# Kernel optimization log

Hardware: AMD Instinct MI355X
Metric: run time of the kernel (lower is better)

The kernel has to match this reference:

```python
import jax, jax.numpy as jnp
import numpy as np

NODE_NUM = 200000   # full-graph embedding table rows
N = 100000          # batch_node_num (unique nodes in batch)
E_RAND = 1_600_000  # random edges (~16/node); self-loops appended -> E = 1.7M
IN_DIM = 256
OUT_DIM = 128
B = 50000           # query nodes
SLOPE = 0.1         # leaky_relu slope_ratio


def setup_inputs() -> dict:
    key = jax.random.key(0)
    k1, k2, k3, k4, k5, k6 = jax.random.split(key, 6)
    features = jax.random.normal(k1, (NODE_NUM, IN_DIM), dtype=jnp.float32)
    W = jax.random.normal(k2, (OUT_DIM, IN_DIM), dtype=jnp.float32) * 0.05
    b = jnp.zeros((OUT_DIM,), dtype=jnp.float32)
    a = jax.random.normal(k3, (2 * OUT_DIM, 1), dtype=jnp.float32) * 0.05
    er = jax.random.randint(k4, (E_RAND, 2), 0, N, dtype=jnp.int64)
    loops = jnp.stack([jnp.arange(N, dtype=jnp.int64)] * 2, axis=1)  # self-loops (original_node_edge)
    edges = jnp.concatenate([er, loops], axis=0)  # [E,2] (src, dst) in unique-node ids
    unique_nodes = jax.random.randint(k5, (N,), 0, NODE_NUM, dtype=jnp.int64)
    node_idx = jax.random.randint(k6, (B,), 0, N, dtype=jnp.int64)
    return {"features": features, "W": W, "b": b, "a": a,
            "edges": edges, "unique_nodes": unique_nodes, "node_idx": node_idx}


def reference(features, W, b, a, edges, unique_nodes, node_idx):
    # new_embeddings = out_linear_layer(features(n2))  -> [N, OUT]
    h = features[unique_nodes] @ W.T + b
    # score per edge: concat(h[src], h[dst]) @ a == h[src]@a_src + h[dst]@a_dst
    a_src = a[:OUT_DIM, 0]
    a_dst = a[OUT_DIM:, 0]
    s_src = h @ a_src  # [N]
    s_dst = h @ a_dst  # [N]
    src, dst = edges[:, 0], edges[:, 1]
    e = jnp.exp(jax.nn.leaky_relu(s_src[src] + s_dst[dst], negative_slope=SLOPE))  # [E]
    # sparse.mm(matrix, new_embeddings) and sparse.mm(matrix, ones) == segment sums over src rows
    num = jax.ops.segment_sum(e[:, None] * h[dst], src, num_segments=N)  # [N, OUT]
    den = jax.ops.segment_sum(e, src, num_segments=N)                    # [N]
    out = num / den[:, None]
    return out[node_idx]
```

## Files before the change

kernel.cpp:

```cpp
#include <hip/hip_runtime.h>

#define IN_DIM   256
#define OUT_DIM  128
#define SLOPE    0.1f

__global__ __launch_bounds__(256) void gemm_h_kernel(
    const float* __restrict__ feat, const float* __restrict__ W,
    const float* __restrict__ bias, const float* __restrict__ avec,
    const int* __restrict__ uniq,
    float* __restrict__ h, float* __restrict__ s_src, float* __restrict__ s_dst,
    int M)
{
  __shared__ float A_lds[32][128];
  __shared__ float B_lds[32][128];
  const int tid = threadIdx.x;
  const int tx = tid & 15, ty = tid >> 4;
  const int m0 = blockIdx.x * 128;
  const int sr = tid & 127;
  const int q  = tid >> 7;

  const int row_s = m0 + sr;
  const int frow = uniq[row_s < M ? row_s : (M - 1)];
  const float* fbase = feat + (size_t)frow * IN_DIM;
  const float* wbase = W + (size_t)sr * IN_DIM;

  float acc[2][2][4][4];
#pragma unroll
  for (int j = 0; j < 2; ++j)
#pragma unroll
    for (int i = 0; i < 2; ++i)
#pragma unroll
      for (int r = 0; r < 4; ++r)
#pragma unroll
        for (int c = 0; c < 4; ++c) acc[j][i][r][c] = 0.f;

  float4 pa[4], pb[4];
#pragma unroll
  for (int p = 0; p < 4; ++p) {
    pa[p] = *(const float4*)(fbase + q * 16 + p * 4);
    pb[p] = *(const float4*)(wbase + q * 16 + p * 4);
  }

  for (int kt = 0; kt < IN_DIM; kt += 32) {
#pragma unroll
    for (int p = 0; p < 4; ++p) {
      const int kk = q * 16 + p * 4;
      A_lds[kk + 0][sr] = pa[p].x; A_lds[kk + 1][sr] = pa[p].y;
      A_lds[kk + 2][sr] = pa[p].z; A_lds[kk + 3][sr] = pa[p].w;
      B_lds[kk + 0][sr] = pb[p].x; B_lds[kk + 1][sr] = pb[p].y;
      B_lds[kk + 2][sr] = pb[p].z; B_lds[kk + 3][sr] = pb[p].w;
    }
    __syncthreads();
    if (kt + 32 < IN_DIM) {
#pragma unroll
      for (int p = 0; p < 4; ++p) {
        pa[p] = *(const float4*)(fbase + kt + 32 + q * 16 + p * 4);
        pb[p] = *(const float4*)(wbase + kt + 32 + q * 16 + p * 4);
      }
    }
#pragma unroll
    for (int kk = 0; kk < 32; ++kk) {
      float4 a0 = *(const float4*)&A_lds[kk][4 * ty];
      float4 a1 = *(const float4*)&A_lds[kk][4 * ty + 64];
      float4 b0 = *(const float4*)&B_lds[kk][4 * tx];
      float4 b1 = *(const float4*)&B_lds[kk][4 * tx + 64];
      float ar[2][4] = {{a0.x, a0.y, a0.z, a0.w}, {a1.x, a1.y, a1.z, a1.w}};
      float br[2][4] = {{b0.x, b0.y, b0.z, b0.w}, {b1.x, b1.y, b1.z, b1.w}};
#pragma unroll
      for (int j = 0; j < 2; ++j)
#pragma unroll
        for (int r = 0; r < 4; ++r)
#pragma unroll
          for (int i = 0; i < 2; ++i)
#pragma unroll
            for (int c = 0; c < 4; ++c)
              acc[j][i][r][c] = fmaf(ar[j][r], br[i][c], acc[j][i][r][c]);
    }
    __syncthreads();
  }

  float4 bb0 = *(const float4*)(bias + 4 * tx);
  float4 bb1 = *(const float4*)(bias + 4 * tx + 64);
  float4 as0 = *(const float4*)(avec + 4 * tx);
  float4 as1 = *(const float4*)(avec + 4 * tx + 64);
  float4 ad0 = *(const float4*)(avec + OUT_DIM + 4 * tx);
  float4 ad1 = *(const float4*)(avec + OUT_DIM + 4 * tx + 64);

#pragma unroll
  for (int j = 0; j < 2; ++j) {
#pragma unroll
    for (int r = 0; r < 4; ++r) {
      const int row = m0 + 4 * ty + 64 * j + r;
      float4 v0, v1;
      v0.x = acc[j][0][r][0] + bb0.x; v0.y = acc[j][0][r][1] + bb0.y;
      v0.z = acc[j][0][r][2] + bb0.z; v0.w = acc[j][0][r][3] + bb0.w;
      v1.x = acc[j][1][r][0] + bb1.x; v1.y = acc[j][1][r][1] + bb1.y;
      v1.z = acc[j][1][r][2] + bb1.z; v1.w = acc[j][1][r][3] + bb1.w;
      float ps = v0.x * as0.x + v0.y * as0.y + v0.z * as0.z + v0.w * as0.w
               + v1.x * as1.x + v1.y * as1.y + v1.z * as1.z + v1.w * as1.w;
      float pd = v0.x * ad0.x + v0.y * ad0.y + v0.z * ad0.z + v0.w * ad0.w
               + v1.x * ad1.x + v1.y * ad1.y + v1.z * ad1.z + v1.w * ad1.w;
#pragma unroll
      for (int d = 1; d < 16; d <<= 1) {
        ps += __shfl_xor(ps, d, 64);
        pd += __shfl_xor(pd, d, 64);
      }
      if (row < M) {
        *(float4*)(h + (size_t)row * OUT_DIM + 4 * tx) = v0;
        *(float4*)(h + (size_t)row * OUT_DIM + 4 * tx + 64) = v1;
        if (tx == 0) { s_src[row] = ps; s_dst[row] = pd; }
      }
    }
  }
}

__global__ __launch_bounds__(256) void hist_kernel(const int* __restrict__ edges,
                                                   const int* __restrict__ nidx,
                                                   int* __restrict__ deg,
                                                   int* __restrict__ odeg,
                                                   int E, int B) {
  int i = blockIdx.x * 256 + threadIdx.x;
  if (i < E) atomicAdd(&deg[((const int2*)edges)[i].x], 1);
  if (i < B) atomicAdd(&odeg[nidx[i]], 1);
}

__global__ __launch_bounds__(256) void scan1_kernel(const int* __restrict__ deg,
                                                    const int* __restrict__ odeg,
                                                    int* __restrict__ bsum,
                                                    int* __restrict__ obsum, int NB) {
  const int tid = threadIdx.x;
  const bool second = blockIdx.x >= NB;
  const int blk = second ? blockIdx.x - NB : blockIdx.x;
  const int* src = second ? odeg : deg;
  int* dst = second ? obsum : bsum;
  const int base = blk * 1024 + tid * 4;
  int4 v = *(const int4*)(src + base);
  int s = v.x + v.y + v.z + v.w;
#pragma unroll
  for (int d = 32; d > 0; d >>= 1) s += __shfl_down(s, d, 64);
  __shared__ int red[4];
  if ((tid & 63) == 0) red[tid >> 6] = s;
  __syncthreads();
  if (tid == 0) dst[blk] = red[0] + red[1] + red[2] + red[3];
}

__global__ __launch_bounds__(256) void scan2_kernel(const int* __restrict__ bsum,
                                                    const int* __restrict__ obsum,
                                                    int* __restrict__ boff,
                                                    int* __restrict__ oboff, int nb,
                                                    int* __restrict__ off_n,
                                                    int* __restrict__ ooff_n) {
  __shared__ int sa[256], sb[256];
  const int tid = threadIdx.x;
  sa[tid] = (tid < nb) ? bsum[tid] : 0;
  sb[tid] = (tid < nb) ? obsum[tid] : 0;
  __syncthreads();
  if (tid == 0) {
    int run = 0;
    for (int i = 0; i < nb; ++i) { int t = sa[i]; boff[i] = run; run += t; }
    *off_n = run;
  }
  if (tid == 64) {
    int run = 0;
    for (int i = 0; i < nb; ++i) { int t = sb[i]; oboff[i] = run; run += t; }
    *ooff_n = run;
  }
}

__global__ __launch_bounds__(256) void scan3_kernel(const int* __restrict__ deg,
                                                    const int* __restrict__ odeg,
                                                    const int* __restrict__ boff,
                                                    const int* __restrict__ oboff,
                                                    int* __restrict__ offs,
                                                    int* __restrict__ ooff,
                                                    int* __restrict__ cursor,
                                                    int* __restrict__ ocur,
                                                    int NB, int n) {
  __shared__ int sh[256];
  const int tid = threadIdx.x;
  const bool second = blockIdx.x >= NB;
  const int blk = second ? blockIdx.x - NB : blockIdx.x;
  const int* src  = second ? odeg : deg;
  const int* bofp = second ? oboff : boff;
  int* offp = second ? ooff : offs;
  int* curp = second ? ocur : cursor;

  const int base = blk * 1024 + tid * 4;
  int4 v = *(const int4*)(src + base);
  const int tot = v.x + v.y + v.z + v.w;
  sh[tid] = tot;
  __syncthreads();
  int run = tot;
#pragma unroll
  for (int st = 1; st < 256; st <<= 1) {
    int other = (tid >= st) ? sh[tid - st] : 0;
    __syncthreads();
    run += other;
    sh[tid] = run;
    __syncthreads();
  }
  int excl = run - tot + bofp[blk];
  int o0 = excl, o1 = o0 + v.x, o2 = o1 + v.y, o3 = o2 + v.z;
  if (base + 0 < n) { offp[base + 0] = o0; curp[base + 0] = o0; }
  if (base + 1 < n) { offp[base + 1] = o1; curp[base + 1] = o1; }
  if (base + 2 < n) { offp[base + 2] = o2; curp[base + 2] = o2; }
  if (base + 3 < n) { offp[base + 3] = o3; curp[base + 3] = o3; }
}

__global__ __launch_bounds__(256) void scatter_kernel(const int* __restrict__ edges,
                                                      const int* __restrict__ nidx,
                                                      int* __restrict__ cursor,
                                                      int* __restrict__ ocur,
                                                      int* __restrict__ csr_dst,
                                                      int* __restrict__ orows,
                                                      int E, int B) {
  int i = blockIdx.x * 256 + threadIdx.x;
  if (i < E) {
    int2 e = ((const int2*)edges)[i];
    int pos = atomicAdd(&cursor[e.x], 1);
    csr_dst[pos] = e.y;
  }
  if (i < B) {
    int n = nidx[i];
    int pos = atomicAdd(&ocur[n], 1);
    orows[pos] = i;
  }
}

__global__ __launch_bounds__(256) void aggregate_kernel(
    const float* __restrict__ h, const float* __restrict__ s_src,
    const float* __restrict__ s_dst, const int* __restrict__ offsets,
    const int* __restrict__ csr_dst, const int* __restrict__ ooff,
    const int* __restrict__ orows, float* __restrict__ out, int N)
{
  const int gw = (blockIdx.x * 256 + threadIdx.x) >> 5;
  const int lane = threadIdx.x & 31;
  if (gw >= N) return;
  const int ob = ooff[gw], oe = ooff[gw + 1];
  if (ob == oe) return;

  const int beg = offsets[gw], end = offsets[gw + 1];
  const float ssrc = s_src[gw];
  const float4* hp = (const float4*)h;

  float ax = 0.f, ay = 0.f, az = 0.f, aw = 0.f, den = 0.f;
  int i = beg;
  for (; i + 4 <= end; i += 4) {
    int d0 = csr_dst[i], d1 = csr_dst[i + 1];
    int d2 = csr_dst[i + 2], d3 = csr_dst[i + 3];
    float z0 = ssrc + s_dst[d0];
    float z1 = ssrc + s_dst[d1];
    float z2 = ssrc + s_dst[d2];
    float z3 = ssrc + s_dst[d3];
    float4 h0 = hp[(size_t)d0 * 32 + lane];
    float4 h1 = hp[(size_t)d1 * 32 + lane];
    float4 h2 = hp[(size_t)d2 * 32 + lane];
    float4 h3 = hp[(size_t)d3 * 32 + lane];
    z0 = z0 > 0.f ? z0 : z0 * SLOPE;
    z1 = z1 > 0.f ? z1 : z1 * SLOPE;
    z2 = z2 > 0.f ? z2 : z2 * SLOPE;
    z3 = z3 > 0.f ? z3 : z3 * SLOPE;
    float e0 = __expf(z0), e1 = __expf(z1);
    float e2 = __expf(z2), e3 = __expf(z3);
    den += (e0 + e1) + (e2 + e3);
    ax = fmaf(e0, h0.x, ax); ay = fmaf(e0, h0.y, ay);
    az = fmaf(e0, h0.z, az); aw = fmaf(e0, h0.w, aw);
    ax = fmaf(e1, h1.x, ax); ay = fmaf(e1, h1.y, ay);
    az = fmaf(e1, h1.z, az); aw = fmaf(e1, h1.w, aw);
    ax = fmaf(e2, h2.x, ax); ay = fmaf(e2, h2.y, ay);
    az = fmaf(e2, h2.z, az); aw = fmaf(e2, h2.w, aw);
    ax = fmaf(e3, h3.x, ax); ay = fmaf(e3, h3.y, ay);
    az = fmaf(e3, h3.z, az); aw = fmaf(e3, h3.w, aw);
  }
  for (; i + 2 <= end; i += 2) {
    int d0 = csr_dst[i], d1 = csr_dst[i + 1];
    float z0 = ssrc + s_dst[d0];
    float z1 = ssrc + s_dst[d1];
    float4 h0 = hp[(size_t)d0 * 32 + lane];
    float4 h1 = hp[(size_t)d1 * 32 + lane];
    z0 = z0 > 0.f ? z0 : z0 * SLOPE;
    z1 = z1 > 0.f ? z1 : z1 * SLOPE;
    float e0 = __expf(z0), e1 = __expf(z1);
    den += e0 + e1;
    ax = fmaf(e0, h0.x, ax); ay = fmaf(e0, h0.y, ay);
    az = fmaf(e0, h0.z, az); aw = fmaf(e0, h0.w, aw);
    ax = fmaf(e1, h1.x, ax); ay = fmaf(e1, h1.y, ay);
    az = fmaf(e1, h1.z, az); aw = fmaf(e1, h1.w, aw);
  }
  if (i < end) {
    int d0 = csr_dst[i];
    float z0 = ssrc + s_dst[d0];
    float4 h0 = hp[(size_t)d0 * 32 + lane];
    z0 = z0 > 0.f ? z0 : z0 * SLOPE;
    float e0 = __expf(z0);
    den += e0;
    ax = fmaf(e0, h0.x, ax); ay = fmaf(e0, h0.y, ay);
    az = fmaf(e0, h0.z, az); aw = fmaf(e0, h0.w, aw);
  }
  const float inv = 1.f / den;
  float4 o; o.x = ax * inv; o.y = ay * inv; o.z = az * inv; o.w = aw * inv;
  for (int j = ob; j < oe; ++j) {
    ((float4*)out)[(size_t)orows[j] * 32 + lane] = o;
  }
}

extern "C" void kernel_launch(void* const* d_in, const int* in_sizes, int n_in,
                              void* d_out, int out_size, void* d_ws, size_t ws_size,
                              hipStream_t stream) {
  const float* feat = (const float*)d_in[0];
  const float* W    = (const float*)d_in[1];
  const float* bias = (const float*)d_in[2];
  const float* avec = (const float*)d_in[3];
  const int*   edges = (const int*)d_in[4];
  const int*   uniq  = (const int*)d_in[5];
  const int*   nidx  = (const int*)d_in[6];
  float* out = (float*)d_out;

  const int E = in_sizes[4] / 2;
  const int N = in_sizes[5];
  const int B = in_sizes[6];
  const int NB   = (N + 1023) / 1024;
  const int NPAD = NB * 1024;

  char* p = (char*)d_ws;
  auto alloc = [&](size_t bytes) -> void* {
    void* r = (void*)p;
    p += (bytes + 511) & ~(size_t)511;
    return r;
  };
  float* h    = (float*)alloc((size_t)N * OUT_DIM * 4);
  float* ssrc = (float*)alloc((size_t)N * 4);
  float* sdst = (float*)alloc((size_t)N * 4);
  int* deg    = (int*)alloc((size_t)2 * NPAD * 4);
  int* odeg   = deg + NPAD;
  int* cursor = (int*)alloc((size_t)N * 4);
  int* ocur   = (int*)alloc((size_t)N * 4);
  int* offs   = (int*)alloc((size_t)(N + 1) * 4);
  int* ooff   = (int*)alloc((size_t)(N + 1) * 4);
  int* bsum   = (int*)alloc((size_t)NB * 4);
  int* obsum  = (int*)alloc((size_t)NB * 4);
  int* boff   = (int*)alloc((size_t)NB * 4);
  int* oboff  = (int*)alloc((size_t)NB * 4);
  int* csr    = (int*)alloc((size_t)E * 4);
  int* orows  = (int*)alloc((size_t)B * 4);

  hipMemsetAsync(deg, 0, (size_t)2 * NPAD * 4, stream);

  gemm_h_kernel<<<(N + 127) / 128, 256, 0, stream>>>(feat, W, bias, avec, uniq,
                                                     h, ssrc, sdst, N);

  hist_kernel<<<(E + 255) / 256, 256, 0, stream>>>(edges, nidx, deg, odeg, E, B);
  scan1_kernel<<<2 * NB, 256, 0, stream>>>(deg, odeg, bsum, obsum, NB);
  scan2_kernel<<<1, 256, 0, stream>>>(bsum, obsum, boff, oboff, NB,
                                      offs + N, ooff + N);
  scan3_kernel<<<2 * NB, 256, 0, stream>>>(deg, odeg, boff, oboff, offs, ooff,
                                           cursor, ocur, NB, N);
  scatter_kernel<<<(E + 255) / 256, 256, 0, stream>>>(edges, nidx, cursor, ocur,
                                                      csr, orows, E, B);

  aggregate_kernel<<<(N * 32 + 255) / 256, 256, 0, stream>>>(h, ssrc, sdst, offs, csr,
                                                             ooff, orows, out, N);
}
```

Measured before the change: 604.5 us.

## Use split-bf16 MFMA for the feature-projection GEMM with prepacked W

Replaces the FP32 SIMT register-tiled GEMM with MFMA 16x16x32 bf16 instructions, splitting each fp32 operand into high and low bf16 parts and using three products to approximate fp32 accuracy. A small pre-kernel packs W into the MFMA operand layout as hi/lo bf16 so the GEMM reads B fragments straight from global memory, and only the gathered feature rows go through LDS. This cuts ALU time in the GEMM stage but adds conversion work, an extra launch, and a small loss of precision from dropping the lo*lo term.

Result: faster. 569.7 us (-5.8%).

```diff
diff --git a/kernel.cpp b/kernel.cpp
--- a/kernel.cpp
+++ b/kernel.cpp
@@ -4,112 +4,125 @@
 #define OUT_DIM  128
 #define SLOPE    0.1f
 
+typedef short short8 __attribute__((ext_vector_type(8)));
+typedef float f32x4  __attribute__((ext_vector_type(4)));
+
+__device__ __forceinline__ void cvt_split8(const float4 a, const float4 b,
+                                           short8& H, short8& L) {
+  float x[8] = {a.x, a.y, a.z, a.w, b.x, b.y, b.z, b.w};
+  short hs[8], ls[8];
+#pragma unroll
+  for (int i = 0; i < 8; ++i) {
+    unsigned u  = __float_as_uint(x[i]);
+    unsigned uh = (u + 0x7FFFu + ((u >> 16) & 1u)) & 0xFFFF0000u;
+    float fh = __uint_as_float(uh);
+    float rl = x[i] - fh;
+    unsigned ul = __float_as_uint(rl);
+    unsigned hl = (ul + 0x7FFFu + ((ul >> 16) & 1u)) >> 16;
+    hs[i] = (short)(uh >> 16);
+    ls[i] = (short)hl;
+  }
+  H = short8{hs[0], hs[1], hs[2], hs[3], hs[4], hs[5], hs[6], hs[7]};
+  L = short8{ls[0], ls[1], ls[2], ls[3], ls[4], ls[5], ls[6], ls[7]};
+}
+
+__global__ __launch_bounds__(256) void wpack_kernel(const float* __restrict__ W,
+                                                    short8* __restrict__ Wh,
+                                                    short8* __restrict__ Wl) {
+  const int slot = blockIdx.x * 256 + threadIdx.x;
+  const int sf = slot >> 6;
+  const int l  = slot & 63;
+  const int col = (sf & 7) * 16 + (l & 15);
+  const int k0  = (sf >> 3) * 32 + (l >> 4) * 8;
+  const float4* p = (const float4*)(W + (size_t)col * IN_DIM + k0);
+  short8 H, L;
+  cvt_split8(p[0], p[1], H, L);
+  Wh[slot] = H;
+  Wl[slot] = L;
+}
+
 __global__ __launch_bounds__(256) void gemm_h_kernel(
-    const float* __restrict__ feat, const float* __restrict__ W,
-    const float* __restrict__ bias, const float* __restrict__ avec,
-    const int* __restrict__ uniq,
+    const float* __restrict__ feat, const short8* __restrict__ Wh,
+    const short8* __restrict__ Wl, const float* __restrict__ bias,
+    const float* __restrict__ avec, const int* __restrict__ uniq,
     float* __restrict__ h, float* __restrict__ s_src, float* __restrict__ s_dst,
     int M)
 {
-  __shared__ float A_lds[32][128];
-  __shared__ float B_lds[32][128];
+  __shared__ short8 Ah[512];
+  __shared__ short8 Al[512];
   const int tid = threadIdx.x;
-  const int tx = tid & 15, ty = tid >> 4;
+  const int w = tid >> 6;
+  const int l = tid & 63;
+  const int c = l & 15, g = l >> 4;
   const int m0 = blockIdx.x * 128;
-  const int sr = tid & 127;
-  const int q  = tid >> 7;
-
-  const int row_s = m0 + sr;
-  const int frow = uniq[row_s < M ? row_s : (M - 1)];
-  const float* fbase = feat + (size_t)frow * IN_DIM;
-  const float* wbase = W + (size_t)sr * IN_DIM;
-
-  float acc[2][2][4][4];
-#pragma unroll
-  for (int j = 0; j < 2; ++j)
-#pragma unroll
-    for (int i = 0; i < 2; ++i)
-#pragma unroll
-      for (int r = 0; r < 4; ++r)
-#pragma unroll
-        for (int c = 0; c < 4; ++c) acc[j][i][r][c] = 0.f;
-
-  float4 pa[4], pb[4];
-#pragma unroll
-  for (int p = 0; p < 4; ++p) {
-    pa[p] = *(const float4*)(fbase + q * 16 + p * 4);
-    pb[p] = *(const float4*)(wbase + q * 16 + p * 4);
-  }
-
-  for (int kt = 0; kt < IN_DIM; kt += 32) {
-#pragma unroll
-    for (int p = 0; p < 4; ++p) {
-      const int kk = q * 16 + p * 4;
-      A_lds[kk + 0][sr] = pa[p].x; A_lds[kk + 1][sr] = pa[p].y;
-      A_lds[kk + 2][sr] = pa[p].z; A_lds[kk + 3][sr] = pa[p].w;
-      B_lds[kk + 0][sr] = pb[p].x; B_lds[kk + 1][sr] = pb[p].y;
-      B_lds[kk + 2][sr] = pb[p].z; B_lds[kk + 3][sr] = pb[p].w;
+
+  const int srow = tid >> 1, kseg = tid & 1;
+  const int frow = uniq[min(m0 + srow, M - 1)];
+  const float4* fb = (const float4*)(feat + (size_t)frow * IN_DIM) + kseg * 4;
+  const int slot0 = (srow >> 4) * 64 + (srow & 15) + 32 * kseg;
+
+  f32x4 acc[2][8] = {};
+
+  float4 pa0 = fb[0], pa1 = fb[1], pa2 = fb[2], pa3 = fb[3];
+  float4 na0, na1, na2, na3;
+
+  for (int s = 0; s < 8; ++s) {
+    short8 H0, L0, H1, L1;
+    cvt_split8(pa0, pa1, H0, L0);
+    cvt_split8(pa2, pa3, H1, L1);
+    Ah[slot0] = H0; Ah[slot0 + 16] = H1;
+    Al[slot0] = L0; Al[slot0 + 16] = L1;
+    __syncthreads();
+    if (s < 7) {
+      const float4* nb = fb + (s + 1) * 8;
+      na0 = nb[0]; na1 = nb[1]; na2 = nb[2]; na3 = nb[3];
+    }
+    short8 a0h = Ah[(w * 2 + 0) * 64 + l], a0l = Al[(w * 2 + 0) * 64 + l];
+    short8 a1h = Ah[(w * 2 + 1) * 64 + l], a1l = Al[(w * 2 + 1) * 64 + l];
+    const short8* wh = Wh + s * 512 + l;
+    const short8* wl = Wl + s * 512 + l;
+#pragma unroll
+    for (int n = 0; n < 8; ++n) {
+      short8 bh = wh[n * 64];
+      short8 bl = wl[n * 64];
+      acc[0][n] = __builtin_amdgcn_mfma_f32_16x16x32_bf16(a0h, bh, acc[0][n], 0, 0, 0);
+      acc[1][n] = __builtin_amdgcn_mfma_f32_16x16x32_bf16(a1h, bh, acc[1][n], 0, 0, 0);
+      acc[0][n] = __builtin_amdgcn_mfma_f32_16x16x32_bf16(a0l, bh, acc[0][n], 0, 0, 0);
+      acc[1][n] = __builtin_amdgcn_mfma_f32_16x16x32_bf16(a1l, bh, acc[1][n], 0, 0, 0);
+      acc[0][n] = __builtin_amdgcn_mfma_f32_16x16x32_bf16(a0h, bl, acc[0][n], 0, 0, 0);
+      acc[1][n] = __builtin_amdgcn_mfma_f32_16x16x32_bf16(a1h, bl, acc[1][n], 0, 0, 0);
     }
     __syncthreads();
-    if (kt + 32 < IN_DIM) {
-#pragma unroll
-      for (int p = 0; p < 4; ++p) {
-        pa[p] = *(const float4*)(fbase + kt + 32 + q * 16 + p * 4);
-        pb[p] = *(const float4*)(wbase + kt + 32 + q * 16 + p * 4);
+    pa0 = na0; pa1 = na1; pa2 = na2; pa3 = na3;
+  }
+
+  float bias_v[8], as_v[8], ad_v[8];
+#pragma unroll
+  for (int n = 0; n < 8; ++n) {
+    bias_v[n] = bias[n * 16 + c];
+    as_v[n]   = avec[n * 16 + c];
+    ad_v[n]   = avec[OUT_DIM + n * 16 + c];
+  }
+#pragma unroll
+  for (int m = 0; m < 2; ++m) {
+#pragma unroll
+    for (int r = 0; r < 4; ++r) {
+      const int grow = m0 + w * 32 + m * 16 + g * 4 + r;
+      const bool ok = grow < M;
+      float ps = 0.f, pd = 0.f;
+#pragma unroll
+      for (int n = 0; n < 8; ++n) {
+        float v = acc[m][n][r] + bias_v[n];
+        if (ok) h[(size_t)grow * OUT_DIM + n * 16 + c] = v;
+        ps = fmaf(v, as_v[n], ps);
+        pd = fmaf(v, ad_v[n], pd);
       }
-    }
-#pragma unroll
-    for (int kk = 0; kk < 32; ++kk) {
-      float4 a0 = *(const float4*)&A_lds[kk][4 * ty];
-      float4 a1 = *(const float4*)&A_lds[kk][4 * ty + 64];
-      float4 b0 = *(const float4*)&B_lds[kk][4 * tx];
-      float4 b1 = *(const float4*)&B_lds[kk][4 * tx + 64];
-      float ar[2][4] = {{a0.x, a0.y, a0.z, a0.w}, {a1.x, a1.y, a1.z, a1.w}};
-      float br[2][4] = {{b0.x, b0.y, b0.z, b0.w}, {b1.x, b1.y, b1.z, b1.w}};
-#pragma unroll
-      for (int j = 0; j < 2; ++j)
-#pragma unroll
-        for (int r = 0; r < 4; ++r)
-#pragma unroll
-          for (int i = 0; i < 2; ++i)
-#pragma unroll
-            for (int c = 0; c < 4; ++c)
-              acc[j][i][r][c] = fmaf(ar[j][r], br[i][c], acc[j][i][r][c]);
-    }
-    __syncthreads();
-  }
-
-  float4 bb0 = *(const float4*)(bias + 4 * tx);
-  float4 bb1 = *(const float4*)(bias + 4 * tx + 64);
-  float4 as0 = *(const float4*)(avec + 4 * tx);
-  float4 as1 = *(const float4*)(avec + 4 * tx + 64);
-  float4 ad0 = *(const float4*)(avec + OUT_DIM + 4 * tx);
-  float4 ad1 = *(const float4*)(avec + OUT_DIM + 4 * tx + 64);
-
-#pragma unroll
-  for (int j = 0; j < 2; ++j) {
-#pragma unroll
-    for (int r = 0; r < 4; ++r) {
-      const int row = m0 + 4 * ty + 64 * j + r;
-      float4 v0, v1;
-      v0.x = acc[j][0][r][0] + bb0.x; v0.y = acc[j][0][r][1] + bb0.y;
-      v0.z = acc[j][0][r][2] + bb0.z; v0.w = acc[j][0][r][3] + bb0.w;
-      v1.x = acc[j][1][r][0] + bb1.x; v1.y = acc[j][1][r][1] + bb1.y;
-      v1.z = acc[j][1][r][2] + bb1.z; v1.w = acc[j][1][r][3] + bb1.w;
-      float ps = v0.x * as0.x + v0.y * as0.y + v0.z * as0.z + v0.w * as0.w
-               + v1.x * as1.x + v1.y * as1.y + v1.z * as1.z + v1.w * as1.w;
-      float pd = v0.x * ad0.x + v0.y * ad0.y + v0.z * ad0.z + v0.w * ad0.w
-               + v1.x * ad1.x + v1.y * ad1.y + v1.z * ad1.z + v1.w * ad1.w;
 #pragma unroll
       for (int d = 1; d < 16; d <<= 1) {
         ps += __shfl_xor(ps, d, 64);
         pd += __shfl_xor(pd, d, 64);
       }
-      if (row < M) {
-        *(float4*)(h + (size_t)row * OUT_DIM + 4 * tx) = v0;
-        *(float4*)(h + (size_t)row * OUT_DIM + 4 * tx + 64) = v1;
-        if (tx == 0) { s_src[row] = ps; s_dst[row] = pd; }
-      }
+      if (ok && c == 0) { s_src[grow] = ps; s_dst[grow] = pd; }
     }
   }
 }
@@ -331,6 +344,8 @@
   float* h    = (float*)alloc((size_t)N * OUT_DIM * 4);
   float* ssrc = (float*)alloc((size_t)N * 4);
   float* sdst = (float*)alloc((size_t)N * 4);
+  short8* Whp = (short8*)alloc((size_t)4096 * 16);
+  short8* Wlp = (short8*)alloc((size_t)4096 * 16);
   int* deg    = (int*)alloc((size_t)2 * NPAD * 4);
   int* odeg   = deg + NPAD;
   int* cursor = (int*)alloc((size_t)N * 4);
@@ -346,8 +361,9 @@
 
   hipMemsetAsync(deg, 0, (size_t)2 * NPAD * 4, stream);
 
-  gemm_h_kernel<<<(N + 127) / 128, 256, 0, stream>>>(feat, W, bias, avec, uniq,
-                                                     h, ssrc, sdst, N);
+  wpack_kernel<<<16, 256, 0, stream>>>(W, Whp, Wlp);
+  gemm_h_kernel<<<(N + 127) / 128, 256, 0, stream>>>(feat, Whp, Wlp, bias, avec,
+                                                     uniq, h, ssrc, sdst, N);
 
   hist_kernel<<<(E + 255) / 256, 256, 0, stream>>>(edges, nidx, deg, odeg, E, B);
   scan1_kernel<<<2 * NB, 256, 0, stream>>>(deg, odeg, bsum, obsum, NB);
```
